# Kernel optimization log

Hardware: AMD Instinct MI355X
Metric: run time of the kernel (lower is better)

Reference implementation:

```python
import math
import jax, jax.numpy as jnp
import numpy as np

HIDDEN = 1024
NUM_HEADS = 16
HEAD_DIM = HIDDEN // NUM_HEADS
B, S = 4, 2048


def setup_inputs() -> dict:
    key = jax.random.key(0)
    ks = jax.random.split(key, 10)
    sc_in = 1.0 / math.sqrt(HIDDEN)
    inp = {
        "query": jax.random.normal(ks[0], (B, S, HIDDEN), jnp.float32),
        "key": jax.random.normal(ks[1], (B, S, HIDDEN), jnp.float32),
        "value": jax.random.normal(ks[2], (B, S, HIDDEN), jnp.float32),
        "mask": jax.random.randint(ks[3], (B, S), 0, 2).astype(bool),
        # NOTE: ModuleList([Linear]*num_heads) shares ONE Linear across all heads.
        "Wq": jax.random.normal(ks[4], (HIDDEN, HEAD_DIM), jnp.float32) * sc_in,
        "bq": jnp.zeros((HEAD_DIM,), jnp.float32),
        "Wk": jax.random.normal(ks[5], (HIDDEN, HEAD_DIM), jnp.float32) * sc_in,
        "bk": jnp.zeros((HEAD_DIM,), jnp.float32),
        "Wv": jax.random.normal(ks[6], (HIDDEN, HEAD_DIM), jnp.float32) * sc_in,
        "bv": jnp.zeros((HEAD_DIM,), jnp.float32),
        "Wout": jax.random.normal(ks[7], (HIDDEN, HIDDEN), jnp.float32) * sc_in,
        "bout": jnp.zeros((HIDDEN,), jnp.float32),
        "seq_mask": 0,
    }
    return inp


def _layer_norm_scores(x, eps=1e-8):
    # torch.std is unbiased (ddof=1); is_train=False => no affine
    mean = jnp.mean(x, axis=-1, keepdims=True)
    sigma = jnp.std(x, axis=-1, keepdims=True, ddof=1)
    return (x - mean) / (sigma + eps)


def reference(query, key, value, mask, Wq, bq, Wk, bk, Wv, bv, Wout, bout, seq_mask):
    # All heads share identical weights -> compute one head, tile the concat.
    q = query @ Wq + bq          # [B,S,hd]
    k = key @ Wk + bk            # [B,S,hd]
    v = value @ Wv + bv          # [B,S,hd]
    scores = jnp.einsum("bqd,bkd->bqk", q, k) / math.sqrt(HIDDEN)  # [B,S,S]
    scores = _layer_norm_scores(scores)
    m = jnp.broadcast_to(mask[:, None, :], scores.shape)  # [B,S,S]
    if seq_mask:
        tri = jnp.triu(jnp.ones(scores.shape[-2:], bool), k=1)
        m = m | tri[None]
    # original fills with -1e-32 (effectively a no-op bug) -- reproduce exactly
    scores = scores + jnp.where(m, jnp.float32(-1e-32), jnp.float32(0.0))
    attn = jax.nn.softmax(scores, axis=-1)
    head = jnp.einsum("bqk,bkd->bqd", attn, v)   # [B,S,hd]
    attention = jnp.tile(head, (1, 1, NUM_HEADS))  # concat of identical heads
    return attention @ Wout + bout
```

## Files before the change

kernel.cpp:

```cpp
#include <hip/hip_runtime.h>
#include <math.h>

#define B_  4
#define S_  2048
#define H_  1024
#define D_  64
#define ROWS (B_*S_)
#define KSPLIT 8
#define LOG2E 1.4426950408889634f

typedef __attribute__((ext_vector_type(4))) float  floatx4;
typedef __attribute__((ext_vector_type(8))) short  short8;
typedef __attribute__((ext_vector_type(8))) __bf16 bf16x8;

#define WS_KSUM 0
#define WS_M    (WS_KSUM + B_*D_)
#define WS_A2   (WS_M + B_*D_*D_)
#define WS_C2   (WS_A2 + ROWS)
#define WS_SWP  (WS_C2 + ROWS)
#define WS_FEND (WS_SWP + KSPLIT*ROWS)
#define WB_QB  0
#define WB_KF  (WB_QB + ROWS*D_)
#define WB_VF  (WB_KF + ROWS*D_)
#define WB_WT  (WB_VF + ROWS*D_)
#define WB_WFF (WB_WT + 3*D_*H_)
#define WB_HNF (WB_WFF + H_*D_)
#define WB_OP  (WB_HNF + ROWS*D_)
#define NZ2    (B_*D_ + B_*D_*D_)

__device__ __forceinline__ unsigned short f2bf(float f) {
    union { float f; unsigned u; } v; v.f = f;
    unsigned r = v.u + 0x7FFFu + ((v.u >> 16) & 1u);
    return (unsigned short)(r >> 16);
}
__device__ __forceinline__ short bfc(float f) {
    __bf16 h = (__bf16)f;
    short s; __builtin_memcpy(&s, &h, 2); return s;
}
__device__ __forceinline__ float bf2f(short s) {
    union { unsigned u; float f; } v;
    v.u = ((unsigned)(unsigned short)s) << 16; return v.f;
}
__device__ __forceinline__ bf16x8 ldb(const short* p) {
    union { short8 s; bf16x8 b; } u; u.s = *(const short8*)p; return u.b;
}
#define MFMA(a,b,c) __builtin_amdgcn_mfma_f32_16x16x32_bf16(a, b, c, 0, 0, 0)
__device__ __forceinline__ void lds_fence() {
    __builtin_amdgcn_wave_barrier();
    __builtin_amdgcn_s_waitcnt(0xc07f);
    __builtin_amdgcn_wave_barrier();
}

__global__ __launch_bounds__(256) void prep(
    const float* __restrict__ Wq, const float* __restrict__ Wk,
    const float* __restrict__ Wv, const float* __restrict__ Wout,
    float* __restrict__ wsf)
{
    __shared__ float tile[64][65];
    short* wsb = (short*)(wsf + WS_FEND);
    const int bx = blockIdx.x, t = threadIdx.x;
    if (bx < 96) {
        int idx = bx * 256 + t;
        int mat = idx >> 13, rem = idx & 8191;
        int kc = rem >> 8, nt = (rem >> 6) & 3, lane = rem & 63;
        int g = lane >> 4, l15 = lane & 15;
        const float* W = (mat == 0) ? Wq : (mat == 1) ? Wk : Wv;
        short8 fr;
        #pragma unroll
        for (int j = 0; j < 8; ++j)
            fr[j] = (short)f2bf(W[(size_t)(kc*32 + g*8 + j) * D_ + nt*16 + l15]);
        *(short8*)&wsb[WB_WT + (size_t)idx * 8] = fr;
    } else if (bx < 112) {
        int n0 = (bx - 96) * 64;
        int nn = t & 63, dg = t >> 6;
        for (int dd = 0; dd < 16; ++dd) {
            int d = dg * 16 + dd;
            float s = 0.0f;
            #pragma unroll
            for (int h = 0; h < 16; ++h)
                s += Wout[(size_t)(h * 64 + d) * H_ + n0 + nn];
            tile[d][nn] = s;
        }
        __syncthreads();
        #pragma unroll
        for (int u = 0; u < 2; ++u) {
            int s = 2*t + u;
            int ctl = s >> 7, h = (s >> 6) & 1, lane = s & 63;
            int g = lane >> 4, l2 = lane & 15;
            short8 fr;
            #pragma unroll
            for (int j = 0; j < 8; ++j)
                fr[j] = (short)f2bf(tile[h*32 + g*8 + j][ctl*16 + l2]);
            *(short8*)&wsb[WB_WFF + (size_t)((((n0 >> 4) + ctl)*2 + h)*64 + lane) * 8] = fr;
        }
    } else {
        int i = (bx - 112) * 256 + t;
        if (i < NZ2) wsf[WS_KSUM + i] = 0.0f;
    }
}

__global__ __launch_bounds__(256) void qkv_mfma(
    const float* __restrict__ query, const float* __restrict__ key,
    const float* __restrict__ value,
    const float* __restrict__ bq, const float* __restrict__ bk,
    const float* __restrict__ bvp, float* __restrict__ wsf)
{
    short* wsb = (short*)(wsf + WS_FEND);
    const int mat = blockIdx.y;
    const float* X    = (mat == 0) ? query : (mat == 1) ? key : value;
    const float* bias = (mat == 0) ? bq    : (mat == 1) ? bk  : bvp;
    const short* WT3 = wsb + WB_WT + (size_t)mat * (D_ * H_);

    const int t = threadIdx.x, w = t >> 6, lane = t & 63;
    const int l15 = lane & 15, g = lane >> 4;
    const int r0 = blockIdx.x * 32;
    const int mrow0 = (w >> 1) * 16;
    const int nt0 = (w & 1) * 2;

    __shared__ short xs[32][136];
    floatx4 acc[2] = {};

    for (int step = 0; step < 8; ++step) {
        __syncthreads();
        #pragma unroll
        for (int u = 0; u < 4; ++u) {
            int row = u * 8 + (t >> 5), col = (t & 31) * 4;
            float4 xv = *(const float4*)&X[(size_t)(r0 + row) * H_ + step * 128 + col];
            short4 pk;
            pk.x = bfc(xv.x); pk.y = bfc(xv.y); pk.z = bfc(xv.z); pk.w = bfc(xv.w);
            *(short4*)&xs[row][col] = pk;
        }
        __syncthreads();
        #pragma unroll
        for (int kk = 0; kk < 4; ++kk) {
            bf16x8 a = ldb(&xs[mrow0 + l15][kk * 32 + g * 8]);
            int kc = step * 4 + kk;
            #pragma unroll
            for (int n = 0; n < 2; ++n) {
                bf16x8 bf = ldb(&WT3[(size_t)((kc * 4) + nt0 + n) * 512 + lane * 8]);
                acc[n] = MFMA(a, bf, acc[n]);
            }
        }
    }

    if (mat == 0) {
        short* QB = wsb + WB_QB;
        #pragma unroll
        for (int n = 0; n < 2; ++n) {
            int col = (nt0 + n) * 16 + l15;
            float bb = bias[col];
            #pragma unroll
            for (int r = 0; r < 4; ++r)
                QB[(size_t)(r0 + mrow0 + 4*g + r) * D_ + col] = (short)f2bf(acc[n][r] + bb);
        }
    } else if (mat == 1) {
        short* KF = wsb + WB_KF;
        #pragma unroll
        for (int n = 0; n < 2; ++n) {
            int d = (nt0 + n) * 16 + l15;
            int kh = d >> 5, gk = (d >> 3) & 3, j = d & 7;
            float bb = bias[d];
            #pragma unroll
            for (int r = 0; r < 4; ++r) {
                int R = r0 + mrow0 + 4*g + r;
                KF[(size_t)(((R >> 4) * 2 + kh) * 64 + gk * 16 + (R & 15)) * 8 + j] =
                    (short)f2bf(acc[n][r] + bb);
            }
        }
    } else {
        short* VF = wsb + WB_VF;
        int R0 = r0 + mrow0 + 4*g;
        int kh = (R0 >> 5) & 1, gv = (R0 >> 3) & 3, j0 = R0 & 7, blk = R0 >> 6;
        #pragma unroll
        for (int n = 0; n < 2; ++n) {
            int d = (nt0 + n) * 16 + l15;
            int ntv = d >> 4;
            float bb = bias[d];
            short4 pk;
            pk.x = (short)f2bf(acc[n][0] + bb); pk.y = (short)f2bf(acc[n][1] + bb);
            pk.z = (short)f2bf(acc[n][2] + bb); pk.w = (short)f2bf(acc[n][3] + bb);
            *(short4*)&VF[(size_t)(((blk * 4 + ntv) * 2 + kh) * 64 + gv * 16 + (d & 15)) * 8 + j0] = pk;
        }
    }
}

__global__ __launch_bounds__(256) void kstats(float* __restrict__ wsf) {
    const short* KF = (short*)(wsf + WS_FEND) + WB_KF;
    const int b     = blockIdx.x >> 5;
    const int chunk = blockIdx.x & 31;
    const int keyblk0 = b * 128 + chunk * 4;

    __shared__ float kt[64][64];
    const int t = threadIdx.x;
    #pragma unroll
    for (int u = 0; u < 2; ++u) {
        int s = 2*t + u;
        int kb4 = s >> 7, kh = (s >> 6) & 1, lane2 = s & 63;
        int g2 = lane2 >> 4, l2 = lane2 & 15;
        short8 v = *(const short8*)&KF[(size_t)(((keyblk0 + kb4) * 2 + kh) * 64 + lane2) * 8];
        #pragma unroll
        for (int j = 0; j < 8; ++j)
            kt[kb4 * 16 + l2][kh * 32 + g2 * 8 + j] = bf2f(v[j]);
    }
    __syncthreads();

    const int td = t >> 4, te = t & 15;
    float acc[4][4] = {};
    for (int j = 0; j < 64; ++j) {
        float4 a  = *(const float4*)&kt[j][td*4];
        float4 bb = *(const float4*)&kt[j][te*4];
        float av[4] = {a.x, a.y, a.z, a.w};
        float bw[4] = {bb.x, bb.y, bb.z, bb.w};
        #pragma unroll
        for (int i = 0; i < 4; ++i)
            #pragma unroll
            for (int l = 0; l < 4; ++l)
                acc[i][l] += av[i] * bw[l];
    }
    float* M = wsf + WS_M + (size_t)b * D_ * D_;
    #pragma unroll
    for (int i = 0; i < 4; ++i)
        #pragma unroll
        for (int l = 0; l < 4; ++l)
            atomicAdd(&M[(td*4 + i) * D_ + te*4 + l], acc[i][l]);

    if (t < 64) {
        float s = 0.0f;
        for (int j = 0; j < 64; ++j) s += kt[j][t];
        atomicAdd(&wsf[WS_KSUM + b * D_ + t], s);
    }
}

__global__ __launch_bounds__(256) void rowstats(float* __restrict__ wsf) {
    const short* Qb = (short*)(wsf + WS_FEND) + WB_QB;
    const int t = threadIdx.x, w = t >> 6, lane = t & 63;
    const int q0 = blockIdx.x * 32 + w * 8;
    const int b  = q0 >> 11;
    const float* M = wsf + WS_M + (size_t)b * D_ * D_;

    float qv[8], y[8] = {};
    #pragma unroll
    for (int r = 0; r < 8; ++r) qv[r] = bf2f(Qb[(size_t)(q0 + r) * D_ + lane]);
    for (int d2 = 0; d2 < 64; ++d2) {
        float m = M[d2 * D_ + lane];
        #pragma unroll
        for (int r = 0; r < 8; ++r) y[r] += __shfl(qv[r], d2, 64) * m;
    }
    float kl = wsf[WS_KSUM + b * D_ + lane];
    float z[8], sv[8];
    #pragma unroll
    for (int r = 0; r < 8; ++r) { z[r] = y[r] * qv[r]; sv[r] = qv[r] * kl; }
    #pragma unroll
    for (int m = 1; m < 64; m <<= 1) {
        #pragma unroll
        for (int r = 0; r < 8; ++r) {
            z[r]  += __shfl_xor(z[r],  m, 64);
            sv[r] += __shfl_xor(sv[r], m, 64);
        }
    }
    #pragma unroll
    for (int r = 0; r < 8; ++r) {
        if (lane == r) {
            float sum   = sv[r] * (1.0f / 32.0f);
            float sumsq = z[r]  * (1.0f / 1024.0f);
            float mu  = sum * (1.0f / 2048.0f);
            float var = (sumsq - sum * sum * (1.0f / 2048.0f)) * (1.0f / 2047.0f);
            var = fmaxf(var, 0.0f);
            float inv = 1.0f / (sqrtf(var) + 1e-8f);
            wsf[WS_A2 + q0 + r] = inv * (LOG2E / 32.0f);
            wsf[WS_C2 + q0 + r] = -mu * inv * LOG2E;
        }
    }
}

__global__ __launch_bounds__(256) void attention(float* __restrict__ wsf) {
    short* wsb = (short*)(wsf + WS_FEND);
    const short* Qb = wsb + WB_QB;
    const short* KF = wsb + WB_KF;
    const short* VF = wsb + WB_VF;
    __shared__ short P[4][32][72];

    const int t = threadIdx.x, w = t >> 6, lane = t & 63;
    const int l15 = lane & 15, g = lane >> 4;
    const int q0 = blockIdx.x * 128 + w * 32;
    const int b  = blockIdx.x >> 4;
    const int kb = blockIdx.y * (S_ / KSPLIT);

    bf16x8 bqf[2][2];
    float a2v[2], c2v[2];
    #pragma unroll
    for (int nt = 0; nt < 2; ++nt) {
        int q = q0 + nt*16 + l15;
        #pragma unroll
        for (int h = 0; h < 2; ++h)
            bqf[nt][h] = ldb(&Qb[(size_t)q * D_ + h*32 + g*8]);
        a2v[nt] = wsf[WS_A2 + q];
        c2v[nt] = wsf[WS_C2 + q];
    }

    floatx4 O[2][4] = {};
    float sacc[2] = {0.0f, 0.0f};
    short* Pw = &P[w][0][0];

    for (int kc = 0; kc < S_ / KSPLIT; kc += 64) {
        const int key0 = kb + kc;
        const int kblk16 = (b * S_ + key0) >> 4;
        const int kblk64 = (b * S_ + key0) >> 6;
        floatx4 Sc[4][2] = {};
        #pragma unroll
        for (int kt = 0; kt < 4; ++kt) {
            bf16x8 ak0 = ldb(&KF[(size_t)(((kblk16 + kt) * 2 + 0) * 64 + lane) * 8]);
            bf16x8 ak1 = ldb(&KF[(size_t)(((kblk16 + kt) * 2 + 1) * 64 + lane) * 8]);
            #pragma unroll
            for (int nt = 0; nt < 2; ++nt) {
                Sc[kt][nt] = MFMA(ak0, bqf[nt][0], Sc[kt][nt]);
                Sc[kt][nt] = MFMA(ak1, bqf[nt][1], Sc[kt][nt]);
            }
        }
        lds_fence();
        #pragma unroll
        for (int nt = 0; nt < 2; ++nt) {
            const float aa = a2v[nt], cc = c2v[nt];
            #pragma unroll
            for (int kt = 0; kt < 4; ++kt) {
                float w0 = exp2f(fmaf(Sc[kt][nt][0], aa, cc));
                float w1 = exp2f(fmaf(Sc[kt][nt][1], aa, cc));
                float w2 = exp2f(fmaf(Sc[kt][nt][2], aa, cc));
                float w3 = exp2f(fmaf(Sc[kt][nt][3], aa, cc));
                sacc[nt] += (w0 + w1) + (w2 + w3);
                short4 pk;
                pk.x = bfc(w0); pk.y = bfc(w1); pk.z = bfc(w2); pk.w = bfc(w3);
                *(short4*)&Pw[(nt*16 + l15) * 72 + kt*16 + 4*g] = pk;
            }
        }
        lds_fence();
        bf16x8 ap[2][2];
        #pragma unroll
        for (int mt = 0; mt < 2; ++mt)
            #pragma unroll
            for (int kh = 0; kh < 2; ++kh)
                ap[mt][kh] = ldb(&Pw[(mt*16 + l15) * 72 + kh*32 + g*8]);
        #pragma unroll
        for (int nt = 0; nt < 4; ++nt) {
            #pragma unroll
            for (int kh = 0; kh < 2; ++kh) {
                bf16x8 bv = ldb(&VF[(size_t)(((kblk64 * 4 + nt) * 2 + kh) * 64 + lane) * 8]);
                #pragma unroll
                for (int mt = 0; mt < 2; ++mt)
                    O[mt][nt] = MFMA(ap[mt][kh], bv, O[mt][nt]);
            }
        }
    }

    #pragma unroll
    for (int nt = 0; nt < 2; ++nt) {
        sacc[nt] += __shfl_xor(sacc[nt], 16, 64);
        sacc[nt] += __shfl_xor(sacc[nt], 32, 64);
    }
    if (lane < 16) {
        wsf[WS_SWP + blockIdx.y * ROWS + q0 + lane]      = sacc[0];
        wsf[WS_SWP + blockIdx.y * ROWS + q0 + 16 + lane] = sacc[1];
    }
    short* OP = wsb + WB_OP + ((size_t)blockIdx.y * ROWS + q0) * D_;
    #pragma unroll
    for (int mt = 0; mt < 2; ++mt)
        #pragma unroll
        for (int nt = 0; nt < 4; ++nt)
            #pragma unroll
            for (int r = 0; r < 4; ++r)
                OP[(size_t)(mt*16 + 4*g + r) * D_ + nt*16 + l15] =
                    (short)f2bf(O[mt][nt][r]);
}

__global__ __launch_bounds__(256) void reduceo(float* __restrict__ wsf) {
    short* wsb = (short*)(wsf + WS_FEND);
    const short* OP = wsb + WB_OP;
    short* HNF = wsb + WB_HNF;
    const int t = threadIdx.x;
    const int row = blockIdx.x * 32 + (t >> 3);
    const int c8 = (t & 7) * 8;
    float sw = 0.0f;
    #pragma unroll
    for (int p = 0; p < KSPLIT; ++p) sw += wsf[WS_SWP + p * ROWS + row];
    float inv = 1.0f / sw;
    float a[8] = {};
    #pragma unroll
    for (int p = 0; p < KSPLIT; ++p) {
        short8 o = *(const short8*)&OP[((size_t)p * ROWS + row) * D_ + c8];
        #pragma unroll
        for (int j = 0; j < 8; ++j) a[j] += bf2f(o[j]);
    }
    short8 hn;
    #pragma unroll
    for (int j = 0; j < 8; ++j) hn[j] = (short)f2bf(a[j] * inv);
    int kh = c8 >> 5, gH = (c8 >> 3) & 3;
    *(short8*)&HNF[(size_t)(((row >> 4) * 2 + kh) * 64 + gH * 16 + (row & 15)) * 8] = hn;
}

__global__ __launch_bounds__(256) void finalize(
    const float* __restrict__ bout, const float* __restrict__ wsf,
    float* __restrict__ out)
{
    const short* wsb = (const short*)(wsf + WS_FEND);
    const short* HNF = wsb + WB_HNF;
    const short* WFF = wsb + WB_WFF;
    const int t = threadIdx.x, w = t >> 6, lane = t & 63;
    const int l15 = lane & 15, g = lane >> 4;
    const int rowblk = blockIdx.x * 4 + w;
    const int r0 = rowblk * 16;
    const int c0 = blockIdx.y * 64;

    bf16x8 ah[2];
    #pragma unroll
    for (int h = 0; h < 2; ++h)
        ah[h] = ldb(&HNF[(size_t)((rowblk * 2 + h) * 64 + lane) * 8]);

    floatx4 acc[4] = {};
    #pragma unroll
    for (int nt = 0; nt < 4; ++nt) {
        #pragma unroll
        for (int h = 0; h < 2; ++h) {
            bf16x8 bf = ldb(&WFF[(size_t)((((c0 >> 4) + nt) * 2 + h) * 64 + lane) * 8]);
            acc[nt] = MFMA(ah[h], bf, acc[nt]);
        }
    }
    #pragma unroll
    for (int nt = 0; nt < 4; ++nt) {
        int col = c0 + nt*16 + l15;
        float bb = bout[col];
        #pragma unroll
        for (int r = 0; r < 4; ++r)
            out[(size_t)(r0 + 4*g + r) * H_ + col] = acc[nt][r] + bb;
    }
}

extern "C" void kernel_launch(void* const* d_in, const int* in_sizes, int n_in,
                              void* d_out, int out_size, void* d_ws, size_t ws_size,
                              hipStream_t stream) {
    const float* query = (const float*)d_in[0];
    const float* key   = (const float*)d_in[1];
    const float* value = (const float*)d_in[2];
    const float* Wq   = (const float*)d_in[4];
    const float* bq   = (const float*)d_in[5];
    const float* Wk   = (const float*)d_in[6];
    const float* bk   = (const float*)d_in[7];
    const float* Wv   = (const float*)d_in[8];
    const float* bv   = (const float*)d_in[9];
    const float* Wout = (const float*)d_in[10];
    const float* bout = (const float*)d_in[11];

    float* ws  = (float*)d_ws;
    float* out = (float*)d_out;

    prep<<<177, 256, 0, stream>>>(Wq, Wk, Wv, Wout, ws);
    qkv_mfma<<<dim3(ROWS/32, 3), 256, 0, stream>>>(query, key, value, bq, bk, bv, ws);
    kstats<<<B_ * 32, 256, 0, stream>>>(ws);
    rowstats<<<ROWS/32, 256, 0, stream>>>(ws);
    attention<<<dim3(ROWS/128, KSPLIT), 256, 0, stream>>>(ws);
    reduceo<<<ROWS/32, 256, 0, stream>>>(ws);
    finalize<<<dim3(ROWS/64, H_/64), 256, 0, stream>>>(bout, ws, out);
}
```

Baseline: 219.5 us.

## Fuse all stages into one cooperative persistent kernel with grid syncs

Merges the seven launches (weight prep, QKV projection, key statistics, row statistics, attention, reduction, output projection) into one cooperative kernel of 512 blocks. Stages are separated by grid-wide barriers, and each block loops over its stage's work items. The QKV tile is also shrunk to 16 rows per block with one MFMA column tile per wave. This removes launch gaps and tail effects between kernels, at the cost of grid-sync overhead and a fixed grid that may underfill some stages, for example the attention stage, which now runs once per block with 512 tiles.

```diff
diff --git a/kernel.cpp b/kernel.cpp
--- a/kernel.cpp
+++ b/kernel.cpp
@@ -1,5 +1,8 @@
 #include <hip/hip_runtime.h>
+#include <hip/hip_cooperative_groups.h>
 #include <math.h>
+
+namespace cg = cooperative_groups;
 
 #define B_  4
 #define S_  2048
@@ -7,6 +10,7 @@
 #define D_  64
 #define ROWS (B_*S_)
 #define KSPLIT 8
+#define GRIDSZ 512
 #define LOG2E 1.4426950408889634f
 
 typedef __attribute__((ext_vector_type(4))) float  floatx4;
@@ -51,386 +55,365 @@
     __builtin_amdgcn_wave_barrier();
 }
 
-__global__ __launch_bounds__(256) void prep(
-    const float* __restrict__ Wq, const float* __restrict__ Wk,
-    const float* __restrict__ Wv, const float* __restrict__ Wout,
-    float* __restrict__ wsf)
-{
-    __shared__ float tile[64][65];
-    short* wsb = (short*)(wsf + WS_FEND);
-    const int bx = blockIdx.x, t = threadIdx.x;
-    if (bx < 96) {
-        int idx = bx * 256 + t;
-        int mat = idx >> 13, rem = idx & 8191;
-        int kc = rem >> 8, nt = (rem >> 6) & 3, lane = rem & 63;
-        int g = lane >> 4, l15 = lane & 15;
-        const float* W = (mat == 0) ? Wq : (mat == 1) ? Wk : Wv;
-        short8 fr;
-        #pragma unroll
-        for (int j = 0; j < 8; ++j)
-            fr[j] = (short)f2bf(W[(size_t)(kc*32 + g*8 + j) * D_ + nt*16 + l15]);
-        *(short8*)&wsb[WB_WT + (size_t)idx * 8] = fr;
-    } else if (bx < 112) {
-        int n0 = (bx - 96) * 64;
-        int nn = t & 63, dg = t >> 6;
-        for (int dd = 0; dd < 16; ++dd) {
-            int d = dg * 16 + dd;
-            float s = 0.0f;
-            #pragma unroll
-            for (int h = 0; h < 16; ++h)
-                s += Wout[(size_t)(h * 64 + d) * H_ + n0 + nn];
-            tile[d][nn] = s;
-        }
-        __syncthreads();
-        #pragma unroll
-        for (int u = 0; u < 2; ++u) {
-            int s = 2*t + u;
-            int ctl = s >> 7, h = (s >> 6) & 1, lane = s & 63;
-            int g = lane >> 4, l2 = lane & 15;
-            short8 fr;
-            #pragma unroll
-            for (int j = 0; j < 8; ++j)
-                fr[j] = (short)f2bf(tile[h*32 + g*8 + j][ctl*16 + l2]);
-            *(short8*)&wsb[WB_WFF + (size_t)((((n0 >> 4) + ctl)*2 + h)*64 + lane) * 8] = fr;
-        }
-    } else {
-        int i = (bx - 112) * 256 + t;
-        if (i < NZ2) wsf[WS_KSUM + i] = 0.0f;
-    }
-}
-
-__global__ __launch_bounds__(256) void qkv_mfma(
+__global__ __launch_bounds__(256, 2) void mega(
     const float* __restrict__ query, const float* __restrict__ key,
     const float* __restrict__ value,
     const float* __restrict__ bq, const float* __restrict__ bk,
-    const float* __restrict__ bvp, float* __restrict__ wsf)
+    const float* __restrict__ bvp,
+    const float* __restrict__ Wq, const float* __restrict__ Wk,
+    const float* __restrict__ Wv, const float* __restrict__ Wout,
+    const float* __restrict__ bout,
+    float* __restrict__ wsf, float* __restrict__ out)
 {
+    cg::grid_group gg = cg::this_grid();
+    __shared__ __align__(16) char smem[18432];
     short* wsb = (short*)(wsf + WS_FEND);
-    const int mat = blockIdx.y;
-    const float* X    = (mat == 0) ? query : (mat == 1) ? key : value;
-    const float* bias = (mat == 0) ? bq    : (mat == 1) ? bk  : bvp;
-    const short* WT3 = wsb + WB_WT + (size_t)mat * (D_ * H_);
 
     const int t = threadIdx.x, w = t >> 6, lane = t & 63;
     const int l15 = lane & 15, g = lane >> 4;
-    const int r0 = blockIdx.x * 32;
-    const int mrow0 = (w >> 1) * 16;
-    const int nt0 = (w & 1) * 2;
-
-    __shared__ short xs[32][136];
-    floatx4 acc[2] = {};
-
-    for (int step = 0; step < 8; ++step) {
-        __syncthreads();
-        #pragma unroll
-        for (int u = 0; u < 4; ++u) {
-            int row = u * 8 + (t >> 5), col = (t & 31) * 4;
-            float4 xv = *(const float4*)&X[(size_t)(r0 + row) * H_ + step * 128 + col];
-            short4 pk;
-            pk.x = bfc(xv.x); pk.y = bfc(xv.y); pk.z = bfc(xv.z); pk.w = bfc(xv.w);
-            *(short4*)&xs[row][col] = pk;
-        }
-        __syncthreads();
-        #pragma unroll
-        for (int kk = 0; kk < 4; ++kk) {
-            bf16x8 a = ldb(&xs[mrow0 + l15][kk * 32 + g * 8]);
-            int kc = step * 4 + kk;
-            #pragma unroll
-            for (int n = 0; n < 2; ++n) {
-                bf16x8 bf = ldb(&WT3[(size_t)((kc * 4) + nt0 + n) * 512 + lane * 8]);
-                acc[n] = MFMA(a, bf, acc[n]);
-            }
-        }
-    }
-
-    if (mat == 0) {
-        short* QB = wsb + WB_QB;
-        #pragma unroll
-        for (int n = 0; n < 2; ++n) {
-            int col = (nt0 + n) * 16 + l15;
+    const int G = GRIDSZ;
+
+    for (int bx = blockIdx.x; bx < 177; bx += G) {
+        if (bx < 96) {
+            int idx = bx * 256 + t;
+            int mat = idx >> 13, rem = idx & 8191;
+            int kc = rem >> 8, nt = (rem >> 6) & 3, ln = rem & 63;
+            int gg2 = ln >> 4, l2 = ln & 15;
+            const float* W = (mat == 0) ? Wq : (mat == 1) ? Wk : Wv;
+            short8 fr;
+            #pragma unroll
+            for (int j = 0; j < 8; ++j)
+                fr[j] = (short)f2bf(W[(size_t)(kc*32 + gg2*8 + j) * D_ + nt*16 + l2]);
+            *(short8*)&wsb[WB_WT + (size_t)idx * 8] = fr;
+        } else if (bx < 112) {
+            float (*tile)[65] = (float(*)[65])smem;
+            int n0 = (bx - 96) * 64;
+            int nn = t & 63, dg = t >> 6;
+            for (int dd = 0; dd < 16; ++dd) {
+                int d = dg * 16 + dd;
+                float s = 0.0f;
+                #pragma unroll
+                for (int h = 0; h < 16; ++h)
+                    s += Wout[(size_t)(h * 64 + d) * H_ + n0 + nn];
+                tile[d][nn] = s;
+            }
+            __syncthreads();
+            #pragma unroll
+            for (int u = 0; u < 2; ++u) {
+                int s = 2*t + u;
+                int ctl = s >> 7, h = (s >> 6) & 1, ln = s & 63;
+                int gg2 = ln >> 4, l2 = ln & 15;
+                short8 fr;
+                #pragma unroll
+                for (int j = 0; j < 8; ++j)
+                    fr[j] = (short)f2bf(tile[h*32 + gg2*8 + j][ctl*16 + l2]);
+                *(short8*)&wsb[WB_WFF + (size_t)((((n0 >> 4) + ctl)*2 + h)*64 + ln) * 8] = fr;
+            }
+        } else {
+            int i = (bx - 112) * 256 + t;
+            if (i < NZ2) wsf[WS_KSUM + i] = 0.0f;
+        }
+    }
+    gg.sync();
+
+    for (int i = blockIdx.x; i < 1536; i += G) {
+        const int mat = i >> 9;
+        const int r0  = (i & 511) * 16;
+        const float* X    = (mat == 0) ? query : (mat == 1) ? key : value;
+        const float* bias = (mat == 0) ? bq    : (mat == 1) ? bk  : bvp;
+        const short* WT3 = wsb + WB_WT + (size_t)mat * (D_ * H_);
+        short (*xs)[136] = (short(*)[136])smem;
+
+        floatx4 acc = {};
+        for (int step = 0; step < 8; ++step) {
+            __syncthreads();
+            #pragma unroll
+            for (int u = 0; u < 2; ++u) {
+                int li = t + u * 256;
+                int row = li >> 5, col = (li & 31) * 4;
+                float4 xv = *(const float4*)&X[(size_t)(r0 + row) * H_ + step * 128 + col];
+                short4 pk;
+                pk.x = bfc(xv.x); pk.y = bfc(xv.y); pk.z = bfc(xv.z); pk.w = bfc(xv.w);
+                *(short4*)&xs[row][col] = pk;
+            }
+            __syncthreads();
+            #pragma unroll
+            for (int kk = 0; kk < 4; ++kk) {
+                bf16x8 a = ldb(&xs[l15][kk * 32 + g * 8]);
+                int kc = step * 4 + kk;
+                bf16x8 bf = ldb(&WT3[(size_t)(kc * 4 + w) * 512 + lane * 8]);
+                acc = MFMA(a, bf, acc);
+            }
+        }
+        if (mat == 0) {
+            short* QB = wsb + WB_QB;
+            int col = w*16 + l15;
             float bb = bias[col];
             #pragma unroll
             for (int r = 0; r < 4; ++r)
-                QB[(size_t)(r0 + mrow0 + 4*g + r) * D_ + col] = (short)f2bf(acc[n][r] + bb);
-        }
-    } else if (mat == 1) {
-        short* KF = wsb + WB_KF;
-        #pragma unroll
-        for (int n = 0; n < 2; ++n) {
-            int d = (nt0 + n) * 16 + l15;
+                QB[(size_t)(r0 + 4*g + r) * D_ + col] = (short)f2bf(acc[r] + bb);
+        } else if (mat == 1) {
+            short* KF = wsb + WB_KF;
+            int d = w*16 + l15;
             int kh = d >> 5, gk = (d >> 3) & 3, j = d & 7;
             float bb = bias[d];
             #pragma unroll
             for (int r = 0; r < 4; ++r) {
-                int R = r0 + mrow0 + 4*g + r;
+                int R = r0 + 4*g + r;
                 KF[(size_t)(((R >> 4) * 2 + kh) * 64 + gk * 16 + (R & 15)) * 8 + j] =
-                    (short)f2bf(acc[n][r] + bb);
-            }
-        }
-    } else {
-        short* VF = wsb + WB_VF;
-        int R0 = r0 + mrow0 + 4*g;
-        int kh = (R0 >> 5) & 1, gv = (R0 >> 3) & 3, j0 = R0 & 7, blk = R0 >> 6;
-        #pragma unroll
-        for (int n = 0; n < 2; ++n) {
-            int d = (nt0 + n) * 16 + l15;
-            int ntv = d >> 4;
+                    (short)f2bf(acc[r] + bb);
+            }
+        } else {
+            short* VF = wsb + WB_VF;
+            int R0 = r0 + 4*g;
+            int kh = (R0 >> 5) & 1, gv = (R0 >> 3) & 3, j0 = R0 & 7, blk = R0 >> 6;
+            int d = w*16 + l15;
             float bb = bias[d];
             short4 pk;
-            pk.x = (short)f2bf(acc[n][0] + bb); pk.y = (short)f2bf(acc[n][1] + bb);
-            pk.z = (short)f2bf(acc[n][2] + bb); pk.w = (short)f2bf(acc[n][3] + bb);
-            *(short4*)&VF[(size_t)(((blk * 4 + ntv) * 2 + kh) * 64 + gv * 16 + (d & 15)) * 8 + j0] = pk;
-        }
-    }
-}
-
-__global__ __launch_bounds__(256) void kstats(float* __restrict__ wsf) {
-    const short* KF = (short*)(wsf + WS_FEND) + WB_KF;
-    const int b     = blockIdx.x >> 5;
-    const int chunk = blockIdx.x & 31;
-    const int keyblk0 = b * 128 + chunk * 4;
-
-    __shared__ float kt[64][64];
-    const int t = threadIdx.x;
-    #pragma unroll
-    for (int u = 0; u < 2; ++u) {
-        int s = 2*t + u;
-        int kb4 = s >> 7, kh = (s >> 6) & 1, lane2 = s & 63;
-        int g2 = lane2 >> 4, l2 = lane2 & 15;
-        short8 v = *(const short8*)&KF[(size_t)(((keyblk0 + kb4) * 2 + kh) * 64 + lane2) * 8];
-        #pragma unroll
-        for (int j = 0; j < 8; ++j)
-            kt[kb4 * 16 + l2][kh * 32 + g2 * 8 + j] = bf2f(v[j]);
-    }
-    __syncthreads();
-
-    const int td = t >> 4, te = t & 15;
-    float acc[4][4] = {};
-    for (int j = 0; j < 64; ++j) {
-        float4 a  = *(const float4*)&kt[j][td*4];
-        float4 bb = *(const float4*)&kt[j][te*4];
-        float av[4] = {a.x, a.y, a.z, a.w};
-        float bw[4] = {bb.x, bb.y, bb.z, bb.w};
-        #pragma unroll
-        for (int i = 0; i < 4; ++i)
+            pk.x = (short)f2bf(acc[0] + bb); pk.y = (short)f2bf(acc[1] + bb);
+            pk.z = (short)f2bf(acc[2] + bb); pk.w = (short)f2bf(acc[3] + bb);
+            *(short4*)&VF[(size_t)(((blk * 4 + w) * 2 + kh) * 64 + gv * 16 + l15) * 8 + j0] = pk;
+        }
+        __syncthreads();
+    }
+    gg.sync();
+
+    for (int bx = blockIdx.x; bx < 128; bx += G) {
+        const short* KF = wsb + WB_KF;
+        const int b = bx >> 5, chunk = bx & 31;
+        const int keyblk0 = b * 128 + chunk * 4;
+        float (*kt)[64] = (float(*)[64])smem;
+        #pragma unroll
+        for (int u = 0; u < 2; ++u) {
+            int s = 2*t + u;
+            int kb4 = s >> 7, kh = (s >> 6) & 1, ln = s & 63;
+            int g2 = ln >> 4, l2 = ln & 15;
+            short8 v = *(const short8*)&KF[(size_t)(((keyblk0 + kb4) * 2 + kh) * 64 + ln) * 8];
+            #pragma unroll
+            for (int j = 0; j < 8; ++j)
+                kt[kb4 * 16 + l2][kh * 32 + g2 * 8 + j] = bf2f(v[j]);
+        }
+        __syncthreads();
+        const int td = t >> 4, te = t & 15;
+        float acc[4][4] = {};
+        for (int j = 0; j < 64; ++j) {
+            float4 a  = *(const float4*)&kt[j][td*4];
+            float4 bb = *(const float4*)&kt[j][te*4];
+            float av[4] = {a.x, a.y, a.z, a.w};
+            float bw[4] = {bb.x, bb.y, bb.z, bb.w};
+            #pragma unroll
+            for (int i2 = 0; i2 < 4; ++i2)
+                #pragma unroll
+                for (int l = 0; l < 4; ++l)
+                    acc[i2][l] += av[i2] * bw[l];
+        }
+        float* M = wsf + WS_M + (size_t)b * D_ * D_;
+        #pragma unroll
+        for (int i2 = 0; i2 < 4; ++i2)
             #pragma unroll
             for (int l = 0; l < 4; ++l)
-                acc[i][l] += av[i] * bw[l];
-    }
-    float* M = wsf + WS_M + (size_t)b * D_ * D_;
-    #pragma unroll
-    for (int i = 0; i < 4; ++i)
-        #pragma unroll
-        for (int l = 0; l < 4; ++l)
-            atomicAdd(&M[(td*4 + i) * D_ + te*4 + l], acc[i][l]);
-
-    if (t < 64) {
-        float s = 0.0f;
-        for (int j = 0; j < 64; ++j) s += kt[j][t];
-        atomicAdd(&wsf[WS_KSUM + b * D_ + t], s);
-    }
-}
-
-__global__ __launch_bounds__(256) void rowstats(float* __restrict__ wsf) {
-    const short* Qb = (short*)(wsf + WS_FEND) + WB_QB;
-    const int t = threadIdx.x, w = t >> 6, lane = t & 63;
-    const int q0 = blockIdx.x * 32 + w * 8;
-    const int b  = q0 >> 11;
-    const float* M = wsf + WS_M + (size_t)b * D_ * D_;
-
-    float qv[8], y[8] = {};
-    #pragma unroll
-    for (int r = 0; r < 8; ++r) qv[r] = bf2f(Qb[(size_t)(q0 + r) * D_ + lane]);
-    for (int d2 = 0; d2 < 64; ++d2) {
-        float m = M[d2 * D_ + lane];
-        #pragma unroll
-        for (int r = 0; r < 8; ++r) y[r] += __shfl(qv[r], d2, 64) * m;
-    }
-    float kl = wsf[WS_KSUM + b * D_ + lane];
-    float z[8], sv[8];
-    #pragma unroll
-    for (int r = 0; r < 8; ++r) { z[r] = y[r] * qv[r]; sv[r] = qv[r] * kl; }
-    #pragma unroll
-    for (int m = 1; m < 64; m <<= 1) {
+                atomicAdd(&M[(td*4 + i2) * D_ + te*4 + l], acc[i2][l]);
+        if (t < 64) {
+            float s = 0.0f;
+            for (int j = 0; j < 64; ++j) s += kt[j][t];
+            atomicAdd(&wsf[WS_KSUM + b * D_ + t], s);
+        }
+        __syncthreads();
+    }
+    gg.sync();
+
+    for (int bx = blockIdx.x; bx < 256; bx += G) {
+        const short* Qb = wsb + WB_QB;
+        const int q0 = bx * 32 + w * 8;
+        const int b  = q0 >> 11;
+        const float* M = wsf + WS_M + (size_t)b * D_ * D_;
+        float qv[8], y[8] = {};
+        #pragma unroll
+        for (int r = 0; r < 8; ++r) qv[r] = bf2f(Qb[(size_t)(q0 + r) * D_ + lane]);
+        for (int d2 = 0; d2 < 64; ++d2) {
+            float m = M[d2 * D_ + lane];
+            #pragma unroll
+            for (int r = 0; r < 8; ++r) y[r] += __shfl(qv[r], d2, 64) * m;
+        }
+        float kl = wsf[WS_KSUM + b * D_ + lane];
+        float z[8], sv[8];
+        #pragma unroll
+        for (int r = 0; r < 8; ++r) { z[r] = y[r] * qv[r]; sv[r] = qv[r] * kl; }
+        #pragma unroll
+        for (int m = 1; m < 64; m <<= 1) {
+            #pragma unroll
+            for (int r = 0; r < 8; ++r) {
+                z[r]  += __shfl_xor(z[r],  m, 64);
+                sv[r] += __shfl_xor(sv[r], m, 64);
+            }
+        }
         #pragma unroll
         for (int r = 0; r < 8; ++r) {
-            z[r]  += __shfl_xor(z[r],  m, 64);
-            sv[r] += __shfl_xor(sv[r], m, 64);
-        }
-    }
-    #pragma unroll
-    for (int r = 0; r < 8; ++r) {
-        if (lane == r) {
-            float sum   = sv[r] * (1.0f / 32.0f);
-            float sumsq = z[r]  * (1.0f / 1024.0f);
-            float mu  = sum * (1.0f / 2048.0f);
-            float var = (sumsq - sum * sum * (1.0f / 2048.0f)) * (1.0f / 2047.0f);
-            var = fmaxf(var, 0.0f);
-            float inv = 1.0f / (sqrtf(var) + 1e-8f);
-            wsf[WS_A2 + q0 + r] = inv * (LOG2E / 32.0f);
-            wsf[WS_C2 + q0 + r] = -mu * inv * LOG2E;
-        }
-    }
-}
-
-__global__ __launch_bounds__(256) void attention(float* __restrict__ wsf) {
-    short* wsb = (short*)(wsf + WS_FEND);
-    const short* Qb = wsb + WB_QB;
-    const short* KF = wsb + WB_KF;
-    const short* VF = wsb + WB_VF;
-    __shared__ short P[4][32][72];
-
-    const int t = threadIdx.x, w = t >> 6, lane = t & 63;
-    const int l15 = lane & 15, g = lane >> 4;
-    const int q0 = blockIdx.x * 128 + w * 32;
-    const int b  = blockIdx.x >> 4;
-    const int kb = blockIdx.y * (S_ / KSPLIT);
-
-    bf16x8 bqf[2][2];
-    float a2v[2], c2v[2];
-    #pragma unroll
-    for (int nt = 0; nt < 2; ++nt) {
-        int q = q0 + nt*16 + l15;
+            if (lane == r) {
+                float sum   = sv[r] * (1.0f / 32.0f);
+                float sumsq = z[r]  * (1.0f / 1024.0f);
+                float mu  = sum * (1.0f / 2048.0f);
+                float var = (sumsq - sum * sum * (1.0f / 2048.0f)) * (1.0f / 2047.0f);
+                var = fmaxf(var, 0.0f);
+                float inv = 1.0f / (sqrtf(var) + 1e-8f);
+                wsf[WS_A2 + q0 + r] = inv * (LOG2E / 32.0f);
+                wsf[WS_C2 + q0 + r] = -mu * inv * LOG2E;
+            }
+        }
+    }
+    gg.sync();
+
+    {
+        const int i = blockIdx.x;
+        const int ax = i & 63, ay = i >> 6;
+        const short* Qb = wsb + WB_QB;
+        const short* KF = wsb + WB_KF;
+        const short* VF = wsb + WB_VF;
+        const int q0 = ax * 128 + w * 32;
+        const int b  = ax >> 4;
+        const int kb = ay * (S_ / KSPLIT);
+        short* Pw = ((short*)smem) + w * (32 * 72);
+
+        bf16x8 bqf[2][2];
+        float a2v[2], c2v[2];
+        #pragma unroll
+        for (int nt = 0; nt < 2; ++nt) {
+            int q = q0 + nt*16 + l15;
+            #pragma unroll
+            for (int h = 0; h < 2; ++h)
+                bqf[nt][h] = ldb(&Qb[(size_t)q * D_ + h*32 + g*8]);
+            a2v[nt] = wsf[WS_A2 + q];
+            c2v[nt] = wsf[WS_C2 + q];
+        }
+
+        floatx4 O[2][4] = {};
+        float sacc[2] = {0.0f, 0.0f};
+
+        for (int kc = 0; kc < S_ / KSPLIT; kc += 64) {
+            const int key0 = kb + kc;
+            const int kblk16 = (b * S_ + key0) >> 4;
+            const int kblk64 = (b * S_ + key0) >> 6;
+            floatx4 Sc[4][2] = {};
+            #pragma unroll
+            for (int kt2 = 0; kt2 < 4; ++kt2) {
+                bf16x8 ak0 = ldb(&KF[(size_t)(((kblk16 + kt2) * 2 + 0) * 64 + lane) * 8]);
+                bf16x8 ak1 = ldb(&KF[(size_t)(((kblk16 + kt2) * 2 + 1) * 64 + lane) * 8]);
+                #pragma unroll
+                for (int nt = 0; nt < 2; ++nt) {
+                    Sc[kt2][nt] = MFMA(ak0, bqf[nt][0], Sc[kt2][nt]);
+                    Sc[kt2][nt] = MFMA(ak1, bqf[nt][1], Sc[kt2][nt]);
+                }
+            }
+            lds_fence();
+            #pragma unroll
+            for (int nt = 0; nt < 2; ++nt) {
+                const float aa = a2v[nt], cc = c2v[nt];
+                #pragma unroll
+                for (int kt2 = 0; kt2 < 4; ++kt2) {
+                    float w0 = exp2f(fmaf(Sc[kt2][nt][0], aa, cc));
+                    float w1 = exp2f(fmaf(Sc[kt2][nt][1], aa, cc));
+                    float w2 = exp2f(fmaf(Sc[kt2][nt][2], aa, cc));
+                    float w3 = exp2f(fmaf(Sc[kt2][nt][3], aa, cc));
+                    sacc[nt] += (w0 + w1) + (w2 + w3);
+                    short4 pk;
+                    pk.x = bfc(w0); pk.y = bfc(w1); pk.z = bfc(w2); pk.w = bfc(w3);
+                    *(short4*)&Pw[(nt*16 + l15) * 72 + kt2*16 + 4*g] = pk;
+                }
+            }
+            lds_fence();
+            bf16x8 ap[2][2];
+            #pragma unroll
+            for (int mt = 0; mt < 2; ++mt)
+                #pragma unroll
+                for (int kh = 0; kh < 2; ++kh)
+                    ap[mt][kh] = ldb(&Pw[(mt*16 + l15) * 72 + kh*32 + g*8]);
+            #pragma unroll
+            for (int nt = 0; nt < 4; ++nt) {
+                #pragma unroll
+                for (int kh = 0; kh < 2; ++kh) {
+                    bf16x8 bv = ldb(&VF[(size_t)(((kblk64 * 4 + nt) * 2 + kh) * 64 + lane) * 8]);
+                    #pragma unroll
+                    for (int mt = 0; mt < 2; ++mt)
+                        O[mt][nt] = MFMA(ap[mt][kh], bv, O[mt][nt]);
+                }
+            }
+        }
+
+        #pragma unroll
+        for (int nt = 0; nt < 2; ++nt) {
+            sacc[nt] += __shfl_xor(sacc[nt], 16, 64);
+            sacc[nt] += __shfl_xor(sacc[nt], 32, 64);
+        }
+        if (lane < 16) {
+            wsf[WS_SWP + ay * ROWS + q0 + lane]      = sacc[0];
+            wsf[WS_SWP + ay * ROWS + q0 + 16 + lane] = sacc[1];
+        }
+        short* OP = wsb + WB_OP + ((size_t)ay * ROWS + q0) * D_;
+        #pragma unroll
+        for (int mt = 0; mt < 2; ++mt)
+            #pragma unroll
+            for (int nt = 0; nt < 4; ++nt)
+                #pragma unroll
+                for (int r = 0; r < 4; ++r)
+                    OP[(size_t)(mt*16 + 4*g + r) * D_ + nt*16 + l15] =
+                        (short)f2bf(O[mt][nt][r]);
+    }
+    gg.sync();
+
+    for (int bx = blockIdx.x; bx < 256; bx += G) {
+        const short* OP = wsb + WB_OP;
+        short* HNF = wsb + WB_HNF;
+        const int row = bx * 32 + (t >> 3);
+        const int c8 = (t & 7) * 8;
+        float sw = 0.0f;
+        #pragma unroll
+        for (int p = 0; p < KSPLIT; ++p) sw += wsf[WS_SWP + p * ROWS + row];
+        float inv = 1.0f / sw;
+        float a[8] = {};
+        #pragma unroll
+        for (int p = 0; p < KSPLIT; ++p) {
+            short8 o = *(const short8*)&OP[((size_t)p * ROWS + row) * D_ + c8];
+            #pragma unroll
+            for (int j = 0; j < 8; ++j) a[j] += bf2f(o[j]);
+        }
+        short8 hn;
+        #pragma unroll
+        for (int j = 0; j < 8; ++j) hn[j] = (short)f2bf(a[j] * inv);
+        int kh = c8 >> 5, gH = (c8 >> 3) & 3;
+        *(short8*)&HNF[(size_t)(((row >> 4) * 2 + kh) * 64 + gH * 16 + (row & 15)) * 8] = hn;
+    }
+    gg.sync();
+
+    for (int i = blockIdx.x; i < 2048; i += G) {
+        const int fx = i & 127, fy = i >> 7;
+        const short* HNF = wsb + WB_HNF;
+        const short* WFF = wsb + WB_WFF;
+        const int rowblk = fx * 4 + w;
+        const int r0 = rowblk * 16;
+        const int c0 = fy * 64;
+
+        bf16x8 ah[2];
         #pragma unroll
         for (int h = 0; h < 2; ++h)
-            bqf[nt][h] = ldb(&Qb[(size_t)q * D_ + h*32 + g*8]);
-        a2v[nt] = wsf[WS_A2 + q];
-        c2v[nt] = wsf[WS_C2 + q];
-    }
-
-    floatx4 O[2][4] = {};
-    float sacc[2] = {0.0f, 0.0f};
-    short* Pw = &P[w][0][0];
-
-    for (int kc = 0; kc < S_ / KSPLIT; kc += 64) {
-        const int key0 = kb + kc;
-        const int kblk16 = (b * S_ + key0) >> 4;
-        const int kblk64 = (b * S_ + key0) >> 6;
-        floatx4 Sc[4][2] = {};
-        #pragma unroll
-        for (int kt = 0; kt < 4; ++kt) {
-            bf16x8 ak0 = ldb(&KF[(size_t)(((kblk16 + kt) * 2 + 0) * 64 + lane) * 8]);
-            bf16x8 ak1 = ldb(&KF[(size_t)(((kblk16 + kt) * 2 + 1) * 64 + lane) * 8]);
-            #pragma unroll
-            for (int nt = 0; nt < 2; ++nt) {
-                Sc[kt][nt] = MFMA(ak0, bqf[nt][0], Sc[kt][nt]);
-                Sc[kt][nt] = MFMA(ak1, bqf[nt][1], Sc[kt][nt]);
-            }
-        }
-        lds_fence();
-        #pragma unroll
-        for (int nt = 0; nt < 2; ++nt) {
-            const float aa = a2v[nt], cc = c2v[nt];
-            #pragma unroll
-            for (int kt = 0; kt < 4; ++kt) {
-                float w0 = exp2f(fmaf(Sc[kt][nt][0], aa, cc));
-                float w1 = exp2f(fmaf(Sc[kt][nt][1], aa, cc));
-                float w2 = exp2f(fmaf(Sc[kt][nt][2], aa, cc));
-                float w3 = exp2f(fmaf(Sc[kt][nt][3], aa, cc));
-                sacc[nt] += (w0 + w1) + (w2 + w3);
-                short4 pk;
-                pk.x = bfc(w0); pk.y = bfc(w1); pk.z = bfc(w2); pk.w = bfc(w3);
-                *(short4*)&Pw[(nt*16 + l15) * 72 + kt*16 + 4*g] = pk;
-            }
-        }
-        lds_fence();
-        bf16x8 ap[2][2];
-        #pragma unroll
-        for (int mt = 0; mt < 2; ++mt)
-            #pragma unroll
-            for (int kh = 0; kh < 2; ++kh)
-                ap[mt][kh] = ldb(&Pw[(mt*16 + l15) * 72 + kh*32 + g*8]);
+            ah[h] = ldb(&HNF[(size_t)((rowblk * 2 + h) * 64 + lane) * 8]);
+
+        floatx4 acc[4] = {};
         #pragma unroll
         for (int nt = 0; nt < 4; ++nt) {
             #pragma unroll
-            for (int kh = 0; kh < 2; ++kh) {
-                bf16x8 bv = ldb(&VF[(size_t)(((kblk64 * 4 + nt) * 2 + kh) * 64 + lane) * 8]);
-                #pragma unroll
-                for (int mt = 0; mt < 2; ++mt)
-                    O[mt][nt] = MFMA(ap[mt][kh], bv, O[mt][nt]);
-            }
-        }
-    }
-
-    #pragma unroll
-    for (int nt = 0; nt < 2; ++nt) {
-        sacc[nt] += __shfl_xor(sacc[nt], 16, 64);
-        sacc[nt] += __shfl_xor(sacc[nt], 32, 64);
-    }
-    if (lane < 16) {
-        wsf[WS_SWP + blockIdx.y * ROWS + q0 + lane]      = sacc[0];
-        wsf[WS_SWP + blockIdx.y * ROWS + q0 + 16 + lane] = sacc[1];
-    }
-    short* OP = wsb + WB_OP + ((size_t)blockIdx.y * ROWS + q0) * D_;
-    #pragma unroll
-    for (int mt = 0; mt < 2; ++mt)
-        #pragma unroll
-        for (int nt = 0; nt < 4; ++nt)
+            for (int h = 0; h < 2; ++h) {
+                bf16x8 bf = ldb(&WFF[(size_t)((((c0 >> 4) + nt) * 2 + h) * 64 + lane) * 8]);
+                acc[nt] = MFMA(ah[h], bf, acc[nt]);
+            }
+        }
+        #pragma unroll
+        for (int nt = 0; nt < 4; ++nt) {
+            int col = c0 + nt*16 + l15;
+            float bb = bout[col];
             #pragma unroll
             for (int r = 0; r < 4; ++r)
-                OP[(size_t)(mt*16 + 4*g + r) * D_ + nt*16 + l15] =
-                    (short)f2bf(O[mt][nt][r]);
-}
-
-__global__ __launch_bounds__(256) void reduceo(float* __restrict__ wsf) {
-    short* wsb = (short*)(wsf + WS_FEND);
-    const short* OP = wsb + WB_OP;
-    short* HNF = wsb + WB_HNF;
-    const int t = threadIdx.x;
-    const int row = blockIdx.x * 32 + (t >> 3);
-    const int c8 = (t & 7) * 8;
-    float sw = 0.0f;
-    #pragma unroll
-    for (int p = 0; p < KSPLIT; ++p) sw += wsf[WS_SWP + p * ROWS + row];
-    float inv = 1.0f / sw;
-    float a[8] = {};
-    #pragma unroll
-    for (int p = 0; p < KSPLIT; ++p) {
-        short8 o = *(const short8*)&OP[((size_t)p * ROWS + row) * D_ + c8];
-        #pragma unroll
-        for (int j = 0; j < 8; ++j) a[j] += bf2f(o[j]);
-    }
-    short8 hn;
-    #pragma unroll
-    for (int j = 0; j < 8; ++j) hn[j] = (short)f2bf(a[j] * inv);
-    int kh = c8 >> 5, gH = (c8 >> 3) & 3;
-    *(short8*)&HNF[(size_t)(((row >> 4) * 2 + kh) * 64 + gH * 16 + (row & 15)) * 8] = hn;
-}
-
-__global__ __launch_bounds__(256) void finalize(
-    const float* __restrict__ bout, const float* __restrict__ wsf,
-    float* __restrict__ out)
-{
-    const short* wsb = (const short*)(wsf + WS_FEND);
-    const short* HNF = wsb + WB_HNF;
-    const short* WFF = wsb + WB_WFF;
-    const int t = threadIdx.x, w = t >> 6, lane = t & 63;
-    const int l15 = lane & 15, g = lane >> 4;
-    const int rowblk = blockIdx.x * 4 + w;
-    const int r0 = rowblk * 16;
-    const int c0 = blockIdx.y * 64;
-
-    bf16x8 ah[2];
-    #pragma unroll
-    for (int h = 0; h < 2; ++h)
-        ah[h] = ldb(&HNF[(size_t)((rowblk * 2 + h) * 64 + lane) * 8]);
-
-    floatx4 acc[4] = {};
-    #pragma unroll
-    for (int nt = 0; nt < 4; ++nt) {
-        #pragma unroll
-        for (int h = 0; h < 2; ++h) {
-            bf16x8 bf = ldb(&WFF[(size_t)((((c0 >> 4) + nt) * 2 + h) * 64 + lane) * 8]);
-            acc[nt] = MFMA(ah[h], bf, acc[nt]);
-        }
-    }
-    #pragma unroll
-    for (int nt = 0; nt < 4; ++nt) {
-        int col = c0 + nt*16 + l15;
-        float bb = bout[col];
-        #pragma unroll
-        for (int r = 0; r < 4; ++r)
-            out[(size_t)(r0 + 4*g + r) * H_ + col] = acc[nt][r] + bb;
+                out[(size_t)(r0 + 4*g + r) * H_ + col] = acc[nt][r] + bb;
+        }
     }
 }
 
@@ -452,11 +435,12 @@
     float* ws  = (float*)d_ws;
     float* out = (float*)d_out;
 
-    prep<<<177, 256, 0, stream>>>(Wq, Wk, Wv, Wout, ws);
-    qkv_mfma<<<dim3(ROWS/32, 3), 256, 0, stream>>>(query, key, value, bq, bk, bv, ws);
-    kstats<<<B_ * 32, 256, 0, stream>>>(ws);
-    rowstats<<<ROWS/32, 256, 0, stream>>>(ws);
-    attention<<<dim3(ROWS/128, KSPLIT), 256, 0, stream>>>(ws);
-    reduceo<<<ROWS/32, 256, 0, stream>>>(ws);
-    finalize<<<dim3(ROWS/64, H_/64), 256, 0, stream>>>(bout, ws, out);
-}
+    void* kargs[] = {
+        (void*)&query, (void*)&key, (void*)&value,
+        (void*)&bq, (void*)&bk, (void*)&bv,
+        (void*)&Wq, (void*)&Wk, (void*)&Wv, (void*)&Wout,
+        (void*)&bout, (void*)&ws, (void*)&out
+    };
+    hipLaunchCooperativeKernel((void*)mega, dim3(GRIDSZ), dim3(256),
+                               kargs, 0, stream);
+}
```

Result: slower. 568.3 us (+158.9%).
